# Kernel tuning notes

Measured on AMD Instinct MI355X. Metric: run time of the kernel, lower is better.

## Reference

```python
import jax, jax.numpy as jnp
import numpy as np

B, N, NODE_DIM, HID, HEAD = 32, 1024, 14, 64, 128
EDGE_PROB = 0.01


def setup_inputs() -> dict:
    key = jax.random.key(0)
    ks = jax.random.split(key, 12)
    x = jax.random.normal(ks[0], (B, N, NODE_DIM), dtype=jnp.float32)
    # sparse binary adjacency with self-loops (matches eye + edge scatter)
    adj = (jax.random.uniform(ks[1], (B, N, N)) < EDGE_PROB).astype(jnp.float32)
    adjacency = jnp.maximum(adj, jnp.eye(N, dtype=jnp.float32)[None])
    def lin(k, din, dout):
        kw, kb = jax.random.split(k)
        w = jax.random.normal(kw, (din, dout), dtype=jnp.float32) / np.sqrt(din)
        b = jnp.zeros((dout,), dtype=jnp.float32)
        return w, b
    W1, b1 = lin(ks[2], NODE_DIM, HID)
    W2, b2 = lin(ks[3], HID, HID)
    W3, b3 = lin(ks[4], HID, HID)
    Wf1, bf1 = lin(ks[5], HID, HEAD)
    Wf2, bf2 = lin(ks[6], HEAD, 1)
    return {"x": x, "adjacency": adjacency, "W1": W1, "b1": b1, "W2": W2,
            "b2": b2, "W3": W3, "b3": b3, "Wf1": Wf1, "bf1": bf1,
            "Wf2": Wf2, "bf2": bf2}


def _dense_graph_conv(x, norm_adj, W, b):
    # (D^-1/2 A D^-1/2) @ x, then linear
    return jnp.einsum('bnm,bmd->bnd', norm_adj, x) @ W + b


def reference(x, adjacency, W1, b1, W2, b2, W3, b3, Wf1, bf1, Wf2, bf2):
    degree = adjacency.sum(axis=-1)                      # [B,N]
    d_inv_sqrt = jnp.clip(degree, 1.0, None) ** -0.5
    norm_adj = d_inv_sqrt[..., :, None] * adjacency * d_inv_sqrt[..., None, :]
    h = jax.nn.relu(_dense_graph_conv(x, norm_adj, W1, b1))
    h = jax.nn.relu(_dense_graph_conv(h, norm_adj, W2, b2))
    h = jax.nn.relu(_dense_graph_conv(h, norm_adj, W3, b3))
    pooled = h.mean(axis=1)                              # [B,HID]
    return jax.nn.relu(pooled @ Wf1 + bf1) @ Wf2 + bf2   # [B,1]
```

## Files before the change

kernel.cpp:

```cpp
#include <hip/hip_runtime.h>
#include <math.h>

#define NN 1024
#define HID 64
#define HEADD 128
#define NODE_DIM 14
#define BATCH 32
#define CAP 64
#define ROWS (BATCH * NN)
#define ZROW ROWS
#define GROW (ROWS + 16)
#define RPW 8

__device__ __forceinline__ int swz4(int blk, int wv) {
    int x = blk & 7, q = blk >> 3;
    int batch = x + 8 * (q >> 8);
    return batch * NN + ((q & 255) << 2) + wv;
}
__device__ __forceinline__ int swz32(int blk, int wv) {
    int x = blk & 7, q = blk >> 3;
    int batch = x + 8 * (q >> 5);
    return batch * NN + ((q & 31) << 5) + wv * RPW;
}

__device__ __forceinline__ float rl_f(float v, int k) {
    return __int_as_float(__builtin_amdgcn_readlane(__float_as_int(v), k));
}

__global__ __launch_bounds__(256) void k_build(const float* __restrict__ adj,
                                               const float* __restrict__ x,
                                               const float* __restrict__ W1,
                                               unsigned short* __restrict__ csr,
                                               int* __restrict__ nnz_g,
                                               float* __restrict__ dinv,
                                               float* __restrict__ g1,
                                               float* __restrict__ g2,
                                               float* __restrict__ g3,
                                               float* __restrict__ pooled) {
    __shared__ float sW1[NODE_DIM * HID];
    for (int i = threadIdx.x; i < NODE_DIM * HID; i += 256) sW1[i] = W1[i];
    if (blockIdx.x < 8) pooled[blockIdx.x * 256 + threadIdx.x] = 0.f;
    if (blockIdx.x == 8 && threadIdx.x < 64) {
        int t = threadIdx.x;
        g1[(size_t)ZROW * HID + t] = 0.f;
        g2[(size_t)ZROW * HID + t] = 0.f;
        g3[(size_t)ZROW * HID + t] = 0.f;
    }
    int wv = threadIdx.x >> 6, lane = threadIdx.x & 63;
    int row = swz4(blockIdx.x, wv);
    int brow = row & ~(NN - 1);
    const float4* rp = reinterpret_cast<const float4*>(adj + (size_t)row * NN);
    unsigned long long lt = ((unsigned long long)1 << lane) - 1;
    int base = 0;
#pragma unroll
    for (int j = 0; j < 4; ++j) {
        float4 v = rp[lane + 64 * j];
        float vv[4] = {v.x, v.y, v.z, v.w};
#pragma unroll
        for (int k = 0; k < 4; ++k) {
            unsigned long long mk = __ballot(vv[k] != 0.0f);
            if (mk) {
                if (vv[k] != 0.0f) {
                    int pos = base + __popcll(mk & lt);
                    if (pos < CAP)
                        csr[row * CAP + pos] =
                            (unsigned short)(brow + (lane + 64 * j) * 4 + k);
                }
                base += __popcll(mk);
            }
        }
    }
    float di = 1.0f / sqrtf((float)(base < 1 ? 1 : base));
    if (lane == 0) {
        nnz_g[row] = base < CAP ? base : CAP;
        dinv[row] = di;
    }
    __syncthreads();
    float acc = 0.f;
    const float* xr = x + (size_t)row * NODE_DIM;
#pragma unroll
    for (int d = 0; d < NODE_DIM; ++d) acc += xr[d] * sW1[d * HID + lane];
    g1[(size_t)row * HID + lane] = acc * di;
}

__device__ __forceinline__ void spmm8(const float* __restrict__ g_in,
                                      const int n[RPW], const int idx[RPW],
                                      unsigned lane, float acc[RPW]) {
    int nmax = 1;
#pragma unroll
    for (int r = 0; r < RPW; ++r) { acc[r] = 0.f; nmax = n[r] > nmax ? n[r] : nmax; }
    float v[RPW];
#pragma unroll
    for (int r = 0; r < RPW; ++r) {
        unsigned j = (unsigned)__builtin_amdgcn_readlane(idx[r], 0);
        v[r] = g_in[j * (unsigned)HID + lane];
    }
    for (int k = 1; k < nmax; ++k) {
        float vn[RPW];
#pragma unroll
        for (int r = 0; r < RPW; ++r) {
            unsigned j = (unsigned)__builtin_amdgcn_readlane(idx[r], k);
            vn[r] = g_in[j * (unsigned)HID + lane];
        }
#pragma unroll
        for (int r = 0; r < RPW; ++r) { acc[r] += v[r]; v[r] = vn[r]; }
    }
#pragma unroll
    for (int r = 0; r < RPW; ++r) acc[r] += v[r];
}

__device__ __forceinline__ void load_meta(const int* __restrict__ nnz_g,
                                          const float* __restrict__ dinv,
                                          const unsigned short* __restrict__ csr,
                                          int row0, int lane,
                                          int n[RPW], int idx[RPW], float dr[RPW]) {
    int nv = nnz_g[row0 + (lane & 7)];
    float dvv = dinv[row0 + (lane & 7)];
#pragma unroll
    for (int r = 0; r < RPW; ++r) {
        n[r] = __builtin_amdgcn_readlane(nv, r);
        dr[r] = rl_f(dvv, r);
    }
#pragma unroll
    for (int r = 0; r < RPW; ++r)
        idx[r] = (lane < n[r]) ? (int)csr[(row0 + r) * CAP + lane] : ZROW;
}

__global__ __launch_bounds__(256, 6) void k_layer(const float* __restrict__ g_in,
                                                  const unsigned short* __restrict__ csr,
                                                  const int* __restrict__ nnz_g,
                                                  const float* __restrict__ dinv,
                                                  const float* __restrict__ bias,
                                                  const float* __restrict__ W,
                                                  float* __restrict__ g_out) {
    __shared__ float sW[HID * HID];
    {
        const float4* Wv = reinterpret_cast<const float4*>(W);
        float4* sWv = reinterpret_cast<float4*>(sW);
        for (int i = threadIdx.x; i < HID * HID / 4; i += 256) sWv[i] = Wv[i];
    }
    int wv = threadIdx.x >> 6, lane = threadIdx.x & 63;
    int row0 = swz32(blockIdx.x, wv);
    float bb = bias[lane];
    int n[RPW], idx[RPW];
    float dr[RPW];
    load_meta(nnz_g, dinv, csr, row0, lane, n, idx, dr);
    float acc[RPW];
    spmm8(g_in, n, idx, (unsigned)lane, acc);
    float h[RPW];
#pragma unroll
    for (int r = 0; r < RPW; ++r)
        h[r] = fmaxf(dr[r] * acc[r] + bb, 0.f) * dr[r];
    __syncthreads();
    float o[RPW];
#pragma unroll
    for (int r = 0; r < RPW; ++r) o[r] = 0.f;
#pragma unroll
    for (int d = 0; d < HID; ++d) {
        float w = sW[d * HID + lane];
#pragma unroll
        for (int r = 0; r < RPW; ++r) o[r] += rl_f(h[r], d) * w;
    }
#pragma unroll
    for (int r = 0; r < RPW; ++r)
        g_out[(size_t)(row0 + r) * HID + lane] = o[r];
}

__global__ __launch_bounds__(256, 6) void k_layer3(const float* __restrict__ g_in,
                                                   const unsigned short* __restrict__ csr,
                                                   const int* __restrict__ nnz_g,
                                                   const float* __restrict__ dinv,
                                                   const float* __restrict__ bias,
                                                   float* __restrict__ pooled) {
    __shared__ float sred[4][HID];
    int wv = threadIdx.x >> 6, lane = threadIdx.x & 63;
    int row0 = swz32(blockIdx.x, wv);
    float bb = bias[lane];
    int n[RPW], idx[RPW];
    float dr[RPW];
    load_meta(nnz_g, dinv, csr, row0, lane, n, idx, dr);
    float acc[RPW];
    spmm8(g_in, n, idx, (unsigned)lane, acc);
    float s = 0.f;
#pragma unroll
    for (int r = 0; r < RPW; ++r)
        s += fmaxf(dr[r] * acc[r] + bb, 0.f);
    sred[wv][lane] = s;
    __syncthreads();
    if (wv == 0) {
        float tot = sred[0][lane] + sred[1][lane] + sred[2][lane] + sred[3][lane];
        atomicAdd(&pooled[(row0 >> 10) * HID + lane], tot);
    }
}

__global__ __launch_bounds__(128) void k_head(const float* __restrict__ pooled_sum,
                                              const float* __restrict__ Wf1,
                                              const float* __restrict__ bf1,
                                              const float* __restrict__ Wf2,
                                              const float* __restrict__ bf2,
                                              float* __restrict__ out) {
    int b = blockIdx.x, t = threadIdx.x;
    __shared__ float p[HID];
    __shared__ float hid[HEADD];
    if (t < HID) p[t] = pooled_sum[b * HID + t] * (1.0f / NN);
    __syncthreads();
    float acc = bf1[t];
    for (int d = 0; d < HID; ++d) acc += p[d] * Wf1[d * HEADD + t];
    hid[t] = fmaxf(acc, 0.f);
    __syncthreads();
    if (t < 64) {
        float v = hid[t] * Wf2[t] + hid[t + 64] * Wf2[t + 64];
#pragma unroll
        for (int off = 32; off > 0; off >>= 1) v += __shfl_down(v, off, 64);
        if (t == 0) out[b] = v + bf2[0];
    }
}

extern "C" void kernel_launch(void* const* d_in, const int* in_sizes, int n_in,
                              void* d_out, int out_size, void* d_ws, size_t ws_size,
                              hipStream_t stream) {
    const float* x   = (const float*)d_in[0];
    const float* adj = (const float*)d_in[1];
    const float* W1  = (const float*)d_in[2];
    const float* b1  = (const float*)d_in[3];
    const float* W2  = (const float*)d_in[4];
    const float* b2  = (const float*)d_in[5];
    const float* W3  = (const float*)d_in[6];
    const float* b3  = (const float*)d_in[7];
    const float* Wf1 = (const float*)d_in[8];
    const float* bf1 = (const float*)d_in[9];
    const float* Wf2 = (const float*)d_in[10];
    const float* bf2 = (const float*)d_in[11];
    float* out = (float*)d_out;

    char* ws = (char*)d_ws;
    size_t off = 0;
    unsigned short* csr = (unsigned short*)(ws + off); off += (size_t)ROWS * CAP * 2;
    int*   nnz_g  = (int*)(ws + off);   off += (size_t)ROWS * 4;
    float* dinv   = (float*)(ws + off); off += (size_t)ROWS * 4;
    float* pooled = (float*)(ws + off); off += 4096 * 4;
    float* g1     = (float*)(ws + off); off += (size_t)GROW * HID * 4;
    float* g2     = (float*)(ws + off); off += (size_t)GROW * HID * 4;
    float* g3     = (float*)(ws + off);

    k_build <<<ROWS / 4, 256, 0, stream>>>(adj, x, W1, csr, nnz_g, dinv, g1, g2, g3, pooled);
    k_layer <<<ROWS / 32, 256, 0, stream>>>(g1, csr, nnz_g, dinv, b1, W2, g2);
    k_layer <<<ROWS / 32, 256, 0, stream>>>(g2, csr, nnz_g, dinv, b2, W3, g3);
    k_layer3<<<ROWS / 32, 256, 0, stream>>>(g3, csr, nnz_g, dinv, b3, pooled);
    k_head  <<<BATCH, 128, 0, stream>>>(pooled, Wf1, bf1, Wf2, bf2, out);
}
```

Measured before the change: 278.0 us.

## Gather neighbor rows as float4 with four neighbors per wave step

After: 275.4 us. Within noise of the previous version (-0.9%).

```diff
diff --git a/kernel.cpp b/kernel.cpp
--- a/kernel.cpp
+++ b/kernel.cpp
@@ -3,6 +3,7 @@
 
 #define NN 1024
 #define HID 64
+#define HID4 16
 #define HEADD 128
 #define NODE_DIM 14
 #define BATCH 32
@@ -70,9 +71,12 @@
             }
         }
     }
+    int nn = base < CAP ? base : CAP;
+    if (lane >= nn)
+        csr[row * CAP + lane] = (unsigned short)ZROW;
     float di = 1.0f / sqrtf((float)(base < 1 ? 1 : base));
     if (lane == 0) {
-        nnz_g[row] = base < CAP ? base : CAP;
+        nnz_g[row] = nn;
         dinv[row] = di;
     }
     __syncthreads();
@@ -83,50 +87,62 @@
     g1[(size_t)row * HID + lane] = acc * di;
 }
 
-__device__ __forceinline__ void spmm8(const float* __restrict__ g_in,
-                                      const int n[RPW], const int idx[RPW],
-                                      unsigned lane, float acc[RPW]) {
-    int nmax = 1;
-#pragma unroll
-    for (int r = 0; r < RPW; ++r) { acc[r] = 0.f; nmax = n[r] > nmax ? n[r] : nmax; }
-    float v[RPW];
-#pragma unroll
-    for (int r = 0; r < RPW; ++r) {
-        unsigned j = (unsigned)__builtin_amdgcn_readlane(idx[r], 0);
-        v[r] = g_in[j * (unsigned)HID + lane];
-    }
-    for (int k = 1; k < nmax; ++k) {
-        float vn[RPW];
-#pragma unroll
-        for (int r = 0; r < RPW; ++r) {
-            unsigned j = (unsigned)__builtin_amdgcn_readlane(idx[r], k);
-            vn[r] = g_in[j * (unsigned)HID + lane];
-        }
-#pragma unroll
-        for (int r = 0; r < RPW; ++r) { acc[r] += v[r]; v[r] = vn[r]; }
-    }
-#pragma unroll
-    for (int r = 0; r < RPW; ++r) acc[r] += v[r];
-}
-
-__device__ __forceinline__ void load_meta(const int* __restrict__ nnz_g,
+__device__ __forceinline__ int load_meta4(const int* __restrict__ nnz_g,
                                           const float* __restrict__ dinv,
                                           const unsigned short* __restrict__ csr,
                                           int row0, int lane,
-                                          int n[RPW], int idx[RPW], float dr[RPW]) {
+                                          int idxv[RPW], float dr[RPW]) {
     int nv = nnz_g[row0 + (lane & 7)];
     float dvv = dinv[row0 + (lane & 7)];
-#pragma unroll
-    for (int r = 0; r < RPW; ++r) {
-        n[r] = __builtin_amdgcn_readlane(nv, r);
+    int nmax = 1;
+#pragma unroll
+    for (int r = 0; r < RPW; ++r) {
+        int nr = __builtin_amdgcn_readlane(nv, r);
+        nmax = nr > nmax ? nr : nmax;
         dr[r] = rl_f(dvv, r);
     }
 #pragma unroll
     for (int r = 0; r < RPW; ++r)
-        idx[r] = (lane < n[r]) ? (int)csr[(row0 + r) * CAP + lane] : ZROW;
-}
-
-__global__ __launch_bounds__(256, 6) void k_layer(const float* __restrict__ g_in,
+        idxv[r] = (int)csr[(row0 + r) * CAP + lane];
+    return (nmax + 3) >> 2;
+}
+
+__device__ __forceinline__ void spmm8v4(const float4* __restrict__ g4,
+                                        int msteps, const int idxv[RPW],
+                                        int g, unsigned s, float4 acc[RPW]) {
+#pragma unroll
+    for (int r = 0; r < RPW; ++r) acc[r] = make_float4(0.f, 0.f, 0.f, 0.f);
+    for (int m = 0; m < msteps; ++m) {
+        int b4 = (m << 2) + g;
+        float4 v[RPW];
+#pragma unroll
+        for (int r = 0; r < RPW; ++r) {
+            unsigned j = (unsigned)__builtin_amdgcn_ds_bpermute(b4 << 2, idxv[r]);
+            v[r] = g4[j * (unsigned)HID4 + s];
+        }
+#pragma unroll
+        for (int r = 0; r < RPW; ++r) {
+            acc[r].x += v[r].x; acc[r].y += v[r].y;
+            acc[r].z += v[r].z; acc[r].w += v[r].w;
+        }
+    }
+}
+
+__device__ __forceinline__ void xreduce(float4 acc[RPW]) {
+#pragma unroll
+    for (int r = 0; r < RPW; ++r) {
+        acc[r].x += __shfl_xor(acc[r].x, 16, 64);
+        acc[r].y += __shfl_xor(acc[r].y, 16, 64);
+        acc[r].z += __shfl_xor(acc[r].z, 16, 64);
+        acc[r].w += __shfl_xor(acc[r].w, 16, 64);
+        acc[r].x += __shfl_xor(acc[r].x, 32, 64);
+        acc[r].y += __shfl_xor(acc[r].y, 32, 64);
+        acc[r].z += __shfl_xor(acc[r].z, 32, 64);
+        acc[r].w += __shfl_xor(acc[r].w, 32, 64);
+    }
+}
+
+__global__ __launch_bounds__(256, 4) void k_layer(const float* __restrict__ g_in,
                                                   const unsigned short* __restrict__ csr,
                                                   const int* __restrict__ nnz_g,
                                                   const float* __restrict__ dinv,
@@ -140,17 +156,24 @@
         for (int i = threadIdx.x; i < HID * HID / 4; i += 256) sWv[i] = Wv[i];
     }
     int wv = threadIdx.x >> 6, lane = threadIdx.x & 63;
+    int g = lane >> 4;
+    unsigned s = (unsigned)(lane & 15);
     int row0 = swz32(blockIdx.x, wv);
-    float bb = bias[lane];
-    int n[RPW], idx[RPW];
+    int idxv[RPW];
     float dr[RPW];
-    load_meta(nnz_g, dinv, csr, row0, lane, n, idx, dr);
-    float acc[RPW];
-    spmm8(g_in, n, idx, (unsigned)lane, acc);
-    float h[RPW];
-#pragma unroll
-    for (int r = 0; r < RPW; ++r)
-        h[r] = fmaxf(dr[r] * acc[r] + bb, 0.f) * dr[r];
+    int msteps = load_meta4(nnz_g, dinv, csr, row0, lane, idxv, dr);
+    float4 acc[RPW];
+    spmm8v4(reinterpret_cast<const float4*>(g_in), msteps, idxv, g, s, acc);
+    xreduce(acc);
+    float4 bb4 = reinterpret_cast<const float4*>(bias)[s];
+    float h_[RPW][4];
+#pragma unroll
+    for (int r = 0; r < RPW; ++r) {
+        h_[r][0] = fmaxf(dr[r] * acc[r].x + bb4.x, 0.f) * dr[r];
+        h_[r][1] = fmaxf(dr[r] * acc[r].y + bb4.y, 0.f) * dr[r];
+        h_[r][2] = fmaxf(dr[r] * acc[r].z + bb4.z, 0.f) * dr[r];
+        h_[r][3] = fmaxf(dr[r] * acc[r].w + bb4.w, 0.f) * dr[r];
+    }
     __syncthreads();
     float o[RPW];
 #pragma unroll
@@ -159,37 +182,53 @@
     for (int d = 0; d < HID; ++d) {
         float w = sW[d * HID + lane];
 #pragma unroll
-        for (int r = 0; r < RPW; ++r) o[r] += rl_f(h[r], d) * w;
+        for (int r = 0; r < RPW; ++r)
+            o[r] += rl_f(h_[r][d & 3], d >> 2) * w;
     }
 #pragma unroll
     for (int r = 0; r < RPW; ++r)
         g_out[(size_t)(row0 + r) * HID + lane] = o[r];
 }
 
-__global__ __launch_bounds__(256, 6) void k_layer3(const float* __restrict__ g_in,
+__global__ __launch_bounds__(256, 4) void k_layer3(const float* __restrict__ g_in,
                                                    const unsigned short* __restrict__ csr,
                                                    const int* __restrict__ nnz_g,
                                                    const float* __restrict__ dinv,
                                                    const float* __restrict__ bias,
                                                    float* __restrict__ pooled) {
-    __shared__ float sred[4][HID];
+    __shared__ float4 sred4[4][HID4];
     int wv = threadIdx.x >> 6, lane = threadIdx.x & 63;
+    int g = lane >> 4;
+    unsigned s = (unsigned)(lane & 15);
     int row0 = swz32(blockIdx.x, wv);
-    float bb = bias[lane];
-    int n[RPW], idx[RPW];
+    int idxv[RPW];
     float dr[RPW];
-    load_meta(nnz_g, dinv, csr, row0, lane, n, idx, dr);
-    float acc[RPW];
-    spmm8(g_in, n, idx, (unsigned)lane, acc);
-    float s = 0.f;
-#pragma unroll
-    for (int r = 0; r < RPW; ++r)
-        s += fmaxf(dr[r] * acc[r] + bb, 0.f);
-    sred[wv][lane] = s;
-    __syncthreads();
-    if (wv == 0) {
-        float tot = sred[0][lane] + sred[1][lane] + sred[2][lane] + sred[3][lane];
-        atomicAdd(&pooled[(row0 >> 10) * HID + lane], tot);
+    int msteps = load_meta4(nnz_g, dinv, csr, row0, lane, idxv, dr);
+    float4 acc[RPW];
+    spmm8v4(reinterpret_cast<const float4*>(g_in), msteps, idxv, g, s, acc);
+    xreduce(acc);
+    float4 bb4 = reinterpret_cast<const float4*>(bias)[s];
+    float4 s4 = make_float4(0.f, 0.f, 0.f, 0.f);
+#pragma unroll
+    for (int r = 0; r < RPW; ++r) {
+        s4.x += fmaxf(dr[r] * acc[r].x + bb4.x, 0.f);
+        s4.y += fmaxf(dr[r] * acc[r].y + bb4.y, 0.f);
+        s4.z += fmaxf(dr[r] * acc[r].z + bb4.z, 0.f);
+        s4.w += fmaxf(dr[r] * acc[r].w + bb4.w, 0.f);
+    }
+    if (lane < 16) sred4[wv][lane] = s4;
+    __syncthreads();
+    if (wv == 0 && lane < 16) {
+        float4 t;
+        t.x = sred4[0][lane].x + sred4[1][lane].x + sred4[2][lane].x + sred4[3][lane].x;
+        t.y = sred4[0][lane].y + sred4[1][lane].y + sred4[2][lane].y + sred4[3][lane].y;
+        t.z = sred4[0][lane].z + sred4[1][lane].z + sred4[2][lane].z + sred4[3][lane].z;
+        t.w = sred4[0][lane].w + sred4[1][lane].w + sred4[2][lane].w + sred4[3][lane].w;
+        float* pb = &pooled[(row0 >> 10) * HID + 4 * lane];
+        atomicAdd(pb + 0, t.x);
+        atomicAdd(pb + 1, t.y);
+        atomicAdd(pb + 2, t.z);
+        atomicAdd(pb + 3, t.w);
     }
 }
 
```
